# Kernel tuning notes

Measured on AMD Instinct MI355X. Metric: run time of the kernel, lower is better.

Reference implementation:

```python
import jax, jax.numpy as jnp
import numpy as np

B, D, K = 8192, 1024, 128
LR = 0.5        # model_args.kmeans_lr, momentum coefficient
EPS = 1e-8      # torch CosineSimilarity eps
NEG_MASK = -10000.0


def setup_inputs() -> dict:
    key = jax.random.key(0)
    k1, k2, k3 = jax.random.split(key, 3)
    return {
        "datapoints": jax.random.normal(k1, (B, D), dtype=jnp.float32),
        "centroid": jax.random.normal(k2, (K, D), dtype=jnp.float32),
        "batch_cos_sim": jax.random.uniform(k3, (B, B), dtype=jnp.float32),
    }


def _cosine_rows(x, y):
    # cosine similarity between every row of x [N,d] and every row of y [M,d]
    xn = x / jnp.maximum(jnp.linalg.norm(x, axis=-1, keepdims=True), EPS)
    yn = y / jnp.maximum(jnp.linalg.norm(y, axis=-1, keepdims=True), EPS)
    return xn @ yn.T  # [N, M]


def reference(datapoints, centroid, batch_cos_sim):
    k = centroid.shape[0]
    b = datapoints.shape[0]

    # cosine sim to centroids (temp = 1)
    intra_cos_sim = _cosine_rows(datapoints, centroid)          # [B, K]

    # hard assignment
    dp_index = jnp.argmax(intra_cos_sim, axis=-1)               # [B]
    onehot = jax.nn.one_hot(dp_index, k, dtype=datapoints.dtype)  # [B, K]

    # intra-class adjacency: same-cluster indicator minus self-loops
    dp_cluster = onehot @ onehot.T - jnp.eye(b, dtype=datapoints.dtype)  # [B, B]

    # gather assigned centroid per datapoint
    dp_centroid = centroid[dp_index]                            # [B, D]

    # hard negative: second-closest centroid
    _, top2_idx = jax.lax.top_k(intra_cos_sim, 2)
    hard_negative = centroid[top2_idx[:, 1]]                    # [B, D]

    # false-negative mask: same-cluster pairs more similar than own centroid
    dp_centroid_cos = jnp.max(intra_cos_sim, axis=-1, keepdims=True)     # [B, 1]
    inter_class_mask = dp_cluster * (batch_cos_sim > dp_centroid_cos)
    cos_mask = inter_class_mask * NEG_MASK                      # [B, B]

    # momentum k-means centroid update
    cluster_sum = onehot.T @ datapoints                         # [K, D]
    updated = (jnp.sum(onehot, axis=0) > 0)[:, None]            # [K, 1] bool
    data = cluster_sum + centroid * (~updated).astype(centroid.dtype)
    new_centroid = LR * data + (1.0 - LR) * centroid            # [K, D]

    return dp_centroid, dp_cluster, hard_negative, cos_mask, new_centroid
```

## Files before the change

kernel.cpp:

```cpp
#include <hip/hip_runtime.h>
#include <cmath>

#define B_N 8192
#define D_N 1024
#define K_N 128


__global__ __launch_bounds__(256) void transpose_cent_k(const float* __restrict__ c,
                                                        float* __restrict__ ct) {
  int e = blockIdx.x * 256 + threadIdx.x;
  int k = e >> 10, d = e & 1023;
  ct[d * K_N + k] = c[e];
}

__global__ __launch_bounds__(256) void norms_k(const float* __restrict__ src,
                                               double* __restrict__ out) {
  int w = threadIdx.x >> 6, lane = threadIdx.x & 63;
  int row = blockIdx.x * 4 + w;
  const float4* s4 = (const float4*)(src + (size_t)row * D_N);
  double acc = 0.0;
#pragma unroll
  for (int e = 0; e < 4; ++e) {
    float4 v = s4[e * 64 + lane];
    acc += (double)v.x * v.x + (double)v.y * v.y + (double)v.z * v.z + (double)v.w * v.w;
  }
#pragma unroll
  for (int off = 32; off; off >>= 1) acc += __shfl_xor(acc, off, 64);
  if (lane == 0) out[row] = acc;
}

__global__ __launch_bounds__(256, 4) void assign_part_k(const float* __restrict__ dp,
                                                        const float* __restrict__ ct,
                                                        float* __restrict__ pdot) {
  __shared__ __align__(16) float xs[32 * 64];
  __shared__ __align__(16) float cs[64 * K_N];
  const int tid = threadIdx.x;
  const int rg = tid >> 5;
  const int cg = tid & 31;
  const int h = blockIdx.x >> 8;
  const int rowbase = (blockIdx.x & 255) * 32;
  const int dbase = h * 256;

  float a32[4][4];
  double a64[4][4];
#pragma unroll
  for (int r = 0; r < 4; ++r)
#pragma unroll
    for (int q = 0; q < 4; ++q) a64[r][q] = 0.0;

  for (int ch = 0; ch < 4; ++ch) {
    const int db = dbase + ch * 64;
#pragma unroll
    for (int i = 0; i < 2; ++i) {
      int fid = tid + i * 256;
      int r = fid >> 4, c4 = (fid & 15) * 4;
      *(float4*)&xs[r * 64 + c4] =
          *(const float4*)&dp[(size_t)(rowbase + r) * D_N + db + c4];
    }
#pragma unroll
    for (int i = 0; i < 8; ++i) {
      int fid = tid + i * 256;
      int dd = fid >> 5, kq = (fid & 31) * 4;
      *(float4*)&cs[dd * K_N + kq] =
          *(const float4*)&ct[(size_t)(db + dd) * K_N + kq];
    }
    __syncthreads();

#pragma unroll
    for (int r = 0; r < 4; ++r)
#pragma unroll
      for (int q = 0; q < 4; ++q) a32[r][q] = 0.0f;

#pragma unroll 2
    for (int dd = 0; dd < 64; dd += 4) {
      float4 cf[4];
#pragma unroll
      for (int e = 0; e < 4; ++e)
        cf[e] = *(const float4*)&cs[(dd + e) * K_N + cg * 4];
#pragma unroll
      for (int r = 0; r < 4; ++r) {
        float4 xv = *(const float4*)&xs[(rg * 4 + r) * 64 + dd];
        a32[r][0] += xv.x * cf[0].x + xv.y * cf[1].x + xv.z * cf[2].x + xv.w * cf[3].x;
        a32[r][1] += xv.x * cf[0].y + xv.y * cf[1].y + xv.z * cf[2].y + xv.w * cf[3].y;
        a32[r][2] += xv.x * cf[0].z + xv.y * cf[1].z + xv.z * cf[2].z + xv.w * cf[3].z;
        a32[r][3] += xv.x * cf[0].w + xv.y * cf[1].w + xv.z * cf[2].w + xv.w * cf[3].w;
      }
    }
#pragma unroll
    for (int r = 0; r < 4; ++r)
#pragma unroll
      for (int q = 0; q < 4; ++q) a64[r][q] += (double)a32[r][q];
    __syncthreads();
  }

  float* base = pdot + (size_t)h * B_N * K_N;
#pragma unroll
  for (int r = 0; r < 4; ++r) {
    int row = rowbase + rg * 4 + r;
    float* o = base + (size_t)row * K_N + cg * 4;
    float4 v = make_float4((float)a64[r][0], (float)a64[r][1],
                           (float)a64[r][2], (float)a64[r][3]);
    *(float4*)o = v;
  }
}

__global__ __launch_bounds__(256) void top2_gather_k(const float* __restrict__ pdot,
                                                     const double* __restrict__ xnorm2,
                                                     const double* __restrict__ cnorm2,
                                                     const float* __restrict__ cent,
                                                     int* __restrict__ dpidx,
                                                     double* __restrict__ maxcos,
                                                     float* __restrict__ out0,
                                                     float* __restrict__ out2) {
  const int w = threadIdx.x >> 6, l = threadIdx.x & 63;
  const int row = blockIdx.x * 4 + w;
  double s0 = 0.0, s1 = 0.0;
#pragma unroll
  for (int h = 0; h < 4; ++h) {
    float2 p = *(const float2*)&pdot[(size_t)h * B_N * K_N + (size_t)row * K_N + 2 * l];
    s0 += (double)p.x; s1 += (double)p.y;
  }
  double xinv = 1.0 / fmax(sqrt(xnorm2[row]), 1e-8);
  double2 cn = *(const double2*)&cnorm2[2 * l];
  double c0 = s0 * xinv / fmax(sqrt(cn.x), 1e-8);
  double c1 = s1 * xinv / fmax(sqrt(cn.y), 1e-8);

  double v1, v2; int i1, i2;
  if (c0 >= c1) { v1 = c0; i1 = 2 * l;     v2 = c1; i2 = 2 * l + 1; }
  else          { v1 = c1; i1 = 2 * l + 1; v2 = c0; i2 = 2 * l; }

#pragma unroll
  for (int off = 1; off < 64; off <<= 1) {
    double pv1 = __shfl_xor(v1, off, 64), pv2 = __shfl_xor(v2, off, 64);
    int    pi1 = __shfl_xor(i1, off, 64), pi2 = __shfl_xor(i2, off, 64);
    bool pb = (pv1 > v1) || (pv1 == v1 && pi1 < i1);
    double w1v = pb ? pv1 : v1;  int w1i = pb ? pi1 : i1;
    double lv  = pb ? v1  : pv1; int li  = pb ? i1  : pi1;
    double sv  = pb ? pv2 : v2;  int si  = pb ? pi2 : i2;
    bool lb = (lv > sv) || (lv == sv && li < si);
    v1 = w1v; i1 = w1i;
    v2 = lb ? lv : sv; i2 = lb ? li : si;
  }
  if (l == 0) { dpidx[row] = i1; maxcos[row] = v1; }

  const float4* g1 = (const float4*)(cent + (size_t)i1 * D_N);
  const float4* g2 = (const float4*)(cent + (size_t)i2 * D_N);
  float4* o0 = (float4*)(out0 + (size_t)row * D_N);
  float4* o2 = (float4*)(out2 + (size_t)row * D_N);
#pragma unroll
  for (int e = 0; e < 4; ++e) {
    o0[e * 64 + l] = g1[e * 64 + l];
    o2[e * 64 + l] = g2[e * 64 + l];
  }
}

__global__ __launch_bounds__(256) void mask_k(const float* __restrict__ batch,
                                              const int* __restrict__ dpidx,
                                              const double* __restrict__ maxcos,
                                              float* __restrict__ out1,
                                              float* __restrict__ out3) {
  const int i = blockIdx.x;
  const int ci = dpidx[i];
  const double thr = maxcos[i];
  const size_t rb = (size_t)i * B_N;
#pragma unroll 2
  for (int it = 0; it < 8; ++it) {
    int j = it * 1024 + threadIdx.x * 4;
    int4 c4 = *(const int4*)&dpidx[j];
    int m0 = (c4.x == ci) & ((j + 0) != i);
    int m1 = (c4.y == ci) & ((j + 1) != i);
    int m2 = (c4.z == ci) & ((j + 2) != i);
    int m3 = (c4.w == ci) & ((j + 3) != i);
    float4 bv = make_float4(0.f, 0.f, 0.f, 0.f);
    if (m0 | m1 | m2 | m3)
      bv = *(const float4*)&batch[rb + j];
    float4 cl = make_float4((float)m0, (float)m1, (float)m2, (float)m3);
    float4 mk = make_float4(
        (m0 && ((double)bv.x > thr)) ? -10000.f : 0.f,
        (m1 && ((double)bv.y > thr)) ? -10000.f : 0.f,
        (m2 && ((double)bv.z > thr)) ? -10000.f : 0.f,
        (m3 && ((double)bv.w > thr)) ? -10000.f : 0.f);
    *(float4*)&out1[rb + j] = cl;
    *(float4*)&out3[rb + j] = mk;
  }
}

__global__ __launch_bounds__(256) void cluster_partial_k(const float* __restrict__ dp,
                                                         const int* __restrict__ dpidx,
                                                         double* __restrict__ psum,
                                                         int* __restrict__ pcnt,
                                                         int nch) {
  const int k = blockIdx.x & 127;
  const int ch = blockIdx.x >> 7;
  const int rows = B_N / nch;
  const int r0 = ch * rows;
  const int t = threadIdx.x;
  double a0 = 0, a1 = 0, a2 = 0, a3 = 0;
  int cnt = 0;
  for (int r = r0; r < r0 + rows; r += 4) {
    int4 q = *(const int4*)&dpidx[r];
    if (q.x == k) { float4 v = *(const float4*)&dp[(size_t)(r + 0) * D_N + t * 4];
                    a0 += v.x; a1 += v.y; a2 += v.z; a3 += v.w; ++cnt; }
    if (q.y == k) { float4 v = *(const float4*)&dp[(size_t)(r + 1) * D_N + t * 4];
                    a0 += v.x; a1 += v.y; a2 += v.z; a3 += v.w; ++cnt; }
    if (q.z == k) { float4 v = *(const float4*)&dp[(size_t)(r + 2) * D_N + t * 4];
                    a0 += v.x; a1 += v.y; a2 += v.z; a3 += v.w; ++cnt; }
    if (q.w == k) { float4 v = *(const float4*)&dp[(size_t)(r + 3) * D_N + t * 4];
                    a0 += v.x; a1 += v.y; a2 += v.z; a3 += v.w; ++cnt; }
  }
  double* o = psum + ((size_t)(ch * 128 + k)) * D_N + t * 4;
  o[0] = a0; o[1] = a1; o[2] = a2; o[3] = a3;
  if (t == 0) pcnt[ch * 128 + k] = cnt;
}

__global__ __launch_bounds__(256) void finalize_k(const float* __restrict__ cent,
                                                  const double* __restrict__ psum,
                                                  const int* __restrict__ pcnt,
                                                  float* __restrict__ out4,
                                                  int nch) {
  int e = blockIdx.x * 256 + threadIdx.x;
  int k = e >> 10;
  int cnt = 0;
  double s = 0.0;
  for (int ch = 0; ch < nch; ++ch) {
    cnt += pcnt[ch * 128 + k];
    s += psum[(size_t)(ch * 128 + k) * D_N + (e & 1023)];
  }
  float c = cent[e];
  out4[e] = (cnt > 0) ? (float)(0.5 * s + 0.5 * (double)c) : c;
}

extern "C" void kernel_launch(void* const* d_in, const int* in_sizes, int n_in,
                              void* d_out, int out_size, void* d_ws, size_t ws_size,
                              hipStream_t stream) {
  const float* dp    = (const float*)d_in[0];
  const float* cent  = (const float*)d_in[1];
  const float* batch = (const float*)d_in[2];

  float* out  = (float*)d_out;
  float* out0 = out;
  float* out1 = out0 + 8388608;
  float* out2 = out1 + 67108864;
  float* out3 = out2 + 8388608;
  float* out4 = out3 + 67108864;

  char* w = (char*)d_ws;
  double* xnorm2 = (double*)(w + 0);
  double* cnorm2 = (double*)(w + 65536);
  int*    dpidx  = (int*)(w + 66560);
  double* maxcos = (double*)(w + 99328);
  float*  ct     = (float*)(w + 164864);
  float*  pdot   = (float*)(w + 689152);
  const size_t psum_base = 689152 + 16777216;

  int nch = 16;
  while (nch > 1 &&
         psum_base + (size_t)nch * (128ull * 1024 * 8 + 128 * 4) > ws_size)
    nch >>= 1;
  double* psum = (double*)(w + psum_base);
  int*    pcnt = (int*)(w + psum_base + (size_t)nch * 128 * 1024 * 8);

  transpose_cent_k<<<dim3(512), dim3(256), 0, stream>>>(cent, ct);
  norms_k<<<dim3(2048), dim3(256), 0, stream>>>(dp, xnorm2);
  norms_k<<<dim3(32), dim3(256), 0, stream>>>(cent, cnorm2);
  assign_part_k<<<dim3(1024), dim3(256), 0, stream>>>(dp, ct, pdot);
  top2_gather_k<<<dim3(2048), dim3(256), 0, stream>>>(pdot, xnorm2, cnorm2, cent,
                                                      dpidx, maxcos, out0, out2);
  mask_k<<<dim3(8192), dim3(256), 0, stream>>>(batch, dpidx, maxcos, out1, out3);
  cluster_partial_k<<<dim3(128 * nch), dim3(256), 0, stream>>>(dp, dpidx, psum, pcnt, nch);
  finalize_k<<<dim3(512), dim3(256), 0, stream>>>(cent, psum, pcnt, out4, nch);
}
```

Before: 261.8 us.

## Fuse prep and mask/cluster kernels, enlarge assign row tile, use nontemporal mask I/O

Merges the centroid transpose and both norm kernels into one launch, and merges the mask kernel with the cluster partial-sum kernel so the two run concurrently in a single grid. The assignment GEMM now processes 64 rows per block (8 rows per thread) with half as many blocks, which increases register reuse of the centroid tile. The mask kernel uses nontemporal loads and stores for the large B×B streams to avoid polluting cache. These changes remove launch gaps and tail idle time, at the cost of higher register pressure and lower occupancy in the assignment kernel.

```diff
diff --git a/kernel.cpp b/kernel.cpp
--- a/kernel.cpp
+++ b/kernel.cpp
@@ -5,18 +5,12 @@
 #define D_N 1024
 #define K_N 128
 
-
-__global__ __launch_bounds__(256) void transpose_cent_k(const float* __restrict__ c,
-                                                        float* __restrict__ ct) {
-  int e = blockIdx.x * 256 + threadIdx.x;
-  int k = e >> 10, d = e & 1023;
-  ct[d * K_N + k] = c[e];
-}
-
-__global__ __launch_bounds__(256) void norms_k(const float* __restrict__ src,
-                                               double* __restrict__ out) {
-  int w = threadIdx.x >> 6, lane = threadIdx.x & 63;
-  int row = blockIdx.x * 4 + w;
+typedef float float4v __attribute__((ext_vector_type(4)));
+
+
+__device__ __forceinline__ void row_norm2(const float* __restrict__ src, int row,
+                                          double* __restrict__ out) {
+  int lane = threadIdx.x & 63;
   const float4* s4 = (const float4*)(src + (size_t)row * D_N);
   double acc = 0.0;
 #pragma unroll
@@ -29,29 +23,48 @@
   if (lane == 0) out[row] = acc;
 }
 
-__global__ __launch_bounds__(256, 4) void assign_part_k(const float* __restrict__ dp,
+__global__ __launch_bounds__(256) void prep_k(const float* __restrict__ dp,
+                                              const float* __restrict__ cent,
+                                              float* __restrict__ ct,
+                                              double* __restrict__ xnorm2,
+                                              double* __restrict__ cnorm2) {
+  int bid = blockIdx.x;
+  if (bid < 512) {
+    int e = bid * 256 + threadIdx.x;
+    int k = e >> 10, d = e & 1023;
+    ct[d * K_N + k] = cent[e];
+  } else if (bid < 2560) {
+    int w = threadIdx.x >> 6;
+    row_norm2(dp, (bid - 512) * 4 + w, xnorm2);
+  } else {
+    int w = threadIdx.x >> 6;
+    row_norm2(cent, (bid - 2560) * 4 + w, cnorm2);
+  }
+}
+
+__global__ __launch_bounds__(256, 3) void assign_part_k(const float* __restrict__ dp,
                                                         const float* __restrict__ ct,
                                                         float* __restrict__ pdot) {
-  __shared__ __align__(16) float xs[32 * 64];
+  __shared__ __align__(16) float xs[64 * 64];
   __shared__ __align__(16) float cs[64 * K_N];
   const int tid = threadIdx.x;
   const int rg = tid >> 5;
   const int cg = tid & 31;
-  const int h = blockIdx.x >> 8;
-  const int rowbase = (blockIdx.x & 255) * 32;
+  const int h = blockIdx.x >> 7;
+  const int rowbase = (blockIdx.x & 127) * 64;
   const int dbase = h * 256;
 
-  float a32[4][4];
-  double a64[4][4];
-#pragma unroll
-  for (int r = 0; r < 4; ++r)
+  float a32[8][4];
+  double a64[8][4];
+#pragma unroll
+  for (int r = 0; r < 8; ++r)
 #pragma unroll
     for (int q = 0; q < 4; ++q) a64[r][q] = 0.0;
 
   for (int ch = 0; ch < 4; ++ch) {
     const int db = dbase + ch * 64;
 #pragma unroll
-    for (int i = 0; i < 2; ++i) {
+    for (int i = 0; i < 4; ++i) {
       int fid = tid + i * 256;
       int r = fid >> 4, c4 = (fid & 15) * 4;
       *(float4*)&xs[r * 64 + c4] =
@@ -67,19 +80,18 @@
     __syncthreads();
 
 #pragma unroll
-    for (int r = 0; r < 4; ++r)
+    for (int r = 0; r < 8; ++r)
 #pragma unroll
       for (int q = 0; q < 4; ++q) a32[r][q] = 0.0f;
 
-#pragma unroll 2
     for (int dd = 0; dd < 64; dd += 4) {
       float4 cf[4];
 #pragma unroll
       for (int e = 0; e < 4; ++e)
         cf[e] = *(const float4*)&cs[(dd + e) * K_N + cg * 4];
 #pragma unroll
-      for (int r = 0; r < 4; ++r) {
-        float4 xv = *(const float4*)&xs[(rg * 4 + r) * 64 + dd];
+      for (int r = 0; r < 8; ++r) {
+        float4 xv = *(const float4*)&xs[(rg * 8 + r) * 64 + dd];
         a32[r][0] += xv.x * cf[0].x + xv.y * cf[1].x + xv.z * cf[2].x + xv.w * cf[3].x;
         a32[r][1] += xv.x * cf[0].y + xv.y * cf[1].y + xv.z * cf[2].y + xv.w * cf[3].y;
         a32[r][2] += xv.x * cf[0].z + xv.y * cf[1].z + xv.z * cf[2].z + xv.w * cf[3].z;
@@ -87,7 +99,7 @@
       }
     }
 #pragma unroll
-    for (int r = 0; r < 4; ++r)
+    for (int r = 0; r < 8; ++r)
 #pragma unroll
       for (int q = 0; q < 4; ++q) a64[r][q] += (double)a32[r][q];
     __syncthreads();
@@ -95,12 +107,11 @@
 
   float* base = pdot + (size_t)h * B_N * K_N;
 #pragma unroll
-  for (int r = 0; r < 4; ++r) {
-    int row = rowbase + rg * 4 + r;
-    float* o = base + (size_t)row * K_N + cg * 4;
+  for (int r = 0; r < 8; ++r) {
+    int row = rowbase + rg * 8 + r;
     float4 v = make_float4((float)a64[r][0], (float)a64[r][1],
                            (float)a64[r][2], (float)a64[r][3]);
-    *(float4*)o = v;
+    *(float4*)(base + (size_t)row * K_N + cg * 4) = v;
   }
 }
 
@@ -154,63 +165,64 @@
   }
 }
 
-__global__ __launch_bounds__(256) void mask_k(const float* __restrict__ batch,
-                                              const int* __restrict__ dpidx,
-                                              const double* __restrict__ maxcos,
-                                              float* __restrict__ out1,
-                                              float* __restrict__ out3) {
-  const int i = blockIdx.x;
-  const int ci = dpidx[i];
-  const double thr = maxcos[i];
-  const size_t rb = (size_t)i * B_N;
+__global__ __launch_bounds__(256) void maskpart_k(const float* __restrict__ batch,
+                                                  const float* __restrict__ dp,
+                                                  const int* __restrict__ dpidx,
+                                                  const double* __restrict__ maxcos,
+                                                  float* __restrict__ out1,
+                                                  float* __restrict__ out3,
+                                                  double* __restrict__ psum,
+                                                  int* __restrict__ pcnt,
+                                                  int nch, int npart) {
+  const int bid = blockIdx.x;
+  const int t = threadIdx.x;
+  if (bid < npart) {
+    const int k = bid & 127;
+    const int ch = bid >> 7;
+    const int rows = B_N / nch;
+    const int r0 = ch * rows;
+    double a0 = 0, a1 = 0, a2 = 0, a3 = 0;
+    int cnt = 0;
+    for (int r = r0; r < r0 + rows; r += 4) {
+      int4 q = *(const int4*)&dpidx[r];
+      if (q.x == k) { float4 v = *(const float4*)&dp[(size_t)(r + 0) * D_N + t * 4];
+                      a0 += v.x; a1 += v.y; a2 += v.z; a3 += v.w; ++cnt; }
+      if (q.y == k) { float4 v = *(const float4*)&dp[(size_t)(r + 1) * D_N + t * 4];
+                      a0 += v.x; a1 += v.y; a2 += v.z; a3 += v.w; ++cnt; }
+      if (q.z == k) { float4 v = *(const float4*)&dp[(size_t)(r + 2) * D_N + t * 4];
+                      a0 += v.x; a1 += v.y; a2 += v.z; a3 += v.w; ++cnt; }
+      if (q.w == k) { float4 v = *(const float4*)&dp[(size_t)(r + 3) * D_N + t * 4];
+                      a0 += v.x; a1 += v.y; a2 += v.z; a3 += v.w; ++cnt; }
+    }
+    double* o = psum + ((size_t)(ch * 128 + k)) * D_N + t * 4;
+    o[0] = a0; o[1] = a1; o[2] = a2; o[3] = a3;
+    if (t == 0) pcnt[ch * 128 + k] = cnt;
+  } else {
+    const int i = bid - npart;
+    const int ci = dpidx[i];
+    const double thr = maxcos[i];
+    const size_t rb = (size_t)i * B_N;
 #pragma unroll 2
-  for (int it = 0; it < 8; ++it) {
-    int j = it * 1024 + threadIdx.x * 4;
-    int4 c4 = *(const int4*)&dpidx[j];
-    int m0 = (c4.x == ci) & ((j + 0) != i);
-    int m1 = (c4.y == ci) & ((j + 1) != i);
-    int m2 = (c4.z == ci) & ((j + 2) != i);
-    int m3 = (c4.w == ci) & ((j + 3) != i);
-    float4 bv = make_float4(0.f, 0.f, 0.f, 0.f);
-    if (m0 | m1 | m2 | m3)
-      bv = *(const float4*)&batch[rb + j];
-    float4 cl = make_float4((float)m0, (float)m1, (float)m2, (float)m3);
-    float4 mk = make_float4(
-        (m0 && ((double)bv.x > thr)) ? -10000.f : 0.f,
-        (m1 && ((double)bv.y > thr)) ? -10000.f : 0.f,
-        (m2 && ((double)bv.z > thr)) ? -10000.f : 0.f,
-        (m3 && ((double)bv.w > thr)) ? -10000.f : 0.f);
-    *(float4*)&out1[rb + j] = cl;
-    *(float4*)&out3[rb + j] = mk;
-  }
-}
-
-__global__ __launch_bounds__(256) void cluster_partial_k(const float* __restrict__ dp,
-                                                         const int* __restrict__ dpidx,
-                                                         double* __restrict__ psum,
-                                                         int* __restrict__ pcnt,
-                                                         int nch) {
-  const int k = blockIdx.x & 127;
-  const int ch = blockIdx.x >> 7;
-  const int rows = B_N / nch;
-  const int r0 = ch * rows;
-  const int t = threadIdx.x;
-  double a0 = 0, a1 = 0, a2 = 0, a3 = 0;
-  int cnt = 0;
-  for (int r = r0; r < r0 + rows; r += 4) {
-    int4 q = *(const int4*)&dpidx[r];
-    if (q.x == k) { float4 v = *(const float4*)&dp[(size_t)(r + 0) * D_N + t * 4];
-                    a0 += v.x; a1 += v.y; a2 += v.z; a3 += v.w; ++cnt; }
-    if (q.y == k) { float4 v = *(const float4*)&dp[(size_t)(r + 1) * D_N + t * 4];
-                    a0 += v.x; a1 += v.y; a2 += v.z; a3 += v.w; ++cnt; }
-    if (q.z == k) { float4 v = *(const float4*)&dp[(size_t)(r + 2) * D_N + t * 4];
-                    a0 += v.x; a1 += v.y; a2 += v.z; a3 += v.w; ++cnt; }
-    if (q.w == k) { float4 v = *(const float4*)&dp[(size_t)(r + 3) * D_N + t * 4];
-                    a0 += v.x; a1 += v.y; a2 += v.z; a3 += v.w; ++cnt; }
-  }
-  double* o = psum + ((size_t)(ch * 128 + k)) * D_N + t * 4;
-  o[0] = a0; o[1] = a1; o[2] = a2; o[3] = a3;
-  if (t == 0) pcnt[ch * 128 + k] = cnt;
+    for (int it = 0; it < 8; ++it) {
+      int j = it * 1024 + t * 4;
+      int4 c4 = *(const int4*)&dpidx[j];
+      int m0 = (c4.x == ci) & ((j + 0) != i);
+      int m1 = (c4.y == ci) & ((j + 1) != i);
+      int m2 = (c4.z == ci) & ((j + 2) != i);
+      int m3 = (c4.w == ci) & ((j + 3) != i);
+      float4v bv = (float4v){0.f, 0.f, 0.f, 0.f};
+      if (m0 | m1 | m2 | m3)
+        bv = __builtin_nontemporal_load((const float4v*)&batch[rb + j]);
+      float4v cl = (float4v){(float)m0, (float)m1, (float)m2, (float)m3};
+      float4v mk = (float4v){
+          (m0 && ((double)bv.x > thr)) ? -10000.f : 0.f,
+          (m1 && ((double)bv.y > thr)) ? -10000.f : 0.f,
+          (m2 && ((double)bv.z > thr)) ? -10000.f : 0.f,
+          (m3 && ((double)bv.w > thr)) ? -10000.f : 0.f};
+      __builtin_nontemporal_store(cl, (float4v*)&out1[rb + j]);
+      __builtin_nontemporal_store(mk, (float4v*)&out3[rb + j]);
+    }
+  }
 }
 
 __global__ __launch_bounds__(256) void finalize_k(const float* __restrict__ cent,
@@ -259,14 +271,14 @@
     nch >>= 1;
   double* psum = (double*)(w + psum_base);
   int*    pcnt = (int*)(w + psum_base + (size_t)nch * 128 * 1024 * 8);
-
-  transpose_cent_k<<<dim3(512), dim3(256), 0, stream>>>(cent, ct);
-  norms_k<<<dim3(2048), dim3(256), 0, stream>>>(dp, xnorm2);
-  norms_k<<<dim3(32), dim3(256), 0, stream>>>(cent, cnorm2);
-  assign_part_k<<<dim3(1024), dim3(256), 0, stream>>>(dp, ct, pdot);
+  const int npart = 128 * nch;
+
+  prep_k<<<dim3(2592), dim3(256), 0, stream>>>(dp, cent, ct, xnorm2, cnorm2);
+  assign_part_k<<<dim3(512), dim3(256), 0, stream>>>(dp, ct, pdot);
   top2_gather_k<<<dim3(2048), dim3(256), 0, stream>>>(pdot, xnorm2, cnorm2, cent,
                                                       dpidx, maxcos, out0, out2);
-  mask_k<<<dim3(8192), dim3(256), 0, stream>>>(batch, dpidx, maxcos, out1, out3);
-  cluster_partial_k<<<dim3(128 * nch), dim3(256), 0, stream>>>(dp, dpidx, psum, pcnt, nch);
+  maskpart_k<<<dim3(npart + 8192), dim3(256), 0, stream>>>(batch, dp, dpidx, maxcos,
+                                                           out1, out3, psum, pcnt,
+                                                           nch, npart);
   finalize_k<<<dim3(512), dim3(256), 0, stream>>>(cent, psum, pcnt, out4, nch);
 }
```

Result: faster. 247.6 us (-5.4%).
